# Kernel optimization log

Measured on AMD Instinct MI355X. Metric: run time of the kernel, lower is better.

## Reference

```python
import jax, jax.numpy as jnp
import numpy as np

B, T, E = 4, 2048, 512
H, D = 8, 64  # num_heads, head_dim


def setup_inputs() -> dict:
    key = jax.random.key(0)
    ks = jax.random.split(key, 9)
    s_in = 1.0 / np.sqrt(E)
    s_pr = 1.0 / np.sqrt(H * D)
    return {
        "x": jax.random.normal(ks[0], (B, T, E), dtype=jnp.float32),
        "Wq": jax.random.uniform(ks[1], (H, E, D), jnp.float32, -s_in, s_in),
        "bq": jax.random.uniform(ks[2], (H, D), jnp.float32, -s_in, s_in),
        "Wk": jax.random.uniform(ks[3], (H, E, D), jnp.float32, -s_in, s_in),
        "bk": jax.random.uniform(ks[4], (H, D), jnp.float32, -s_in, s_in),
        "Wv": jax.random.uniform(ks[5], (H, E, D), jnp.float32, -s_in, s_in),
        "bv": jax.random.uniform(ks[6], (H, D), jnp.float32, -s_in, s_in),
        "Wp": jax.random.uniform(ks[7], (H * D, E), jnp.float32, -s_pr, s_pr),
        "bp": jax.random.uniform(ks[8], (E,), jnp.float32, -s_pr, s_pr),
    }


def reference(x, Wq, bq, Wk, bk, Wv, bv, Wp, bp):
    # Per-head projections, vectorized over heads: [B,T,E] x [H,E,D] -> [B,H,T,D]
    Q = jnp.einsum('bte,hed->bhtd', x, Wq) + bq[None, :, None, :]
    K = jnp.einsum('bte,hed->bhtd', x, Wk) + bk[None, :, None, :]
    V = jnp.einsum('bte,hed->bhtd', x, Wv) + bv[None, :, None, :]
    scale = 1.0 / jnp.sqrt(jnp.float32(D))
    att = jnp.einsum('bhtd,bhsd->bhts', Q, K) * scale  # [B,H,T,T]
    causal = jnp.tril(jnp.ones((T, T), dtype=bool))
    att = jnp.where(causal[None, None], att, -jnp.inf)
    att = jax.nn.softmax(att, axis=-1)
    out = jnp.einsum('bhts,bhsd->bhtd', att, V)  # [B,H,T,D]
    # concat heads: [B,T,H*D]
    out = out.transpose(0, 2, 1, 3).reshape(B, T, H * D)
    return out @ Wp + bp
```

## Files before the change

### kernel.cpp

```cpp
#include <hip/hip_runtime.h>
#include <hip/hip_bf16.h>

typedef unsigned short u16;
typedef __bf16 bf16x8 __attribute__((ext_vector_type(8)));
typedef float f32x4 __attribute__((ext_vector_type(4)));

#define B_ 4
#define T_ 2048
#define E_ 512
#define H_ 8
#define D_ 64
#define M_ (B_*T_)
#define NQKV (3*H_*D_)

__device__ __forceinline__ u16 f2b(float f) {
  unsigned u = __float_as_uint(f);
  return (u16)((u + 0x7fffu + ((u >> 16) & 1u)) >> 16);
}

__device__ __forceinline__ void gl_lds16(const void* g, void* l) {
  __builtin_amdgcn_global_load_lds((const __attribute__((address_space(1))) void*)g,
                                   (__attribute__((address_space(3))) void*)l, 16, 0, 0);
}

__global__ void k_prep(const float* __restrict__ x, u16* __restrict__ xb,
                       const float* __restrict__ Wq, const float* __restrict__ Wk,
                       const float* __restrict__ Wv, u16* __restrict__ wt,
                       const float* __restrict__ Wp, u16* __restrict__ wpT) {
  int bid = blockIdx.x;
  if (bid < 4096) {
    int i = bid * 256 + threadIdx.x;
    float4 v = reinterpret_cast<const float4*>(x)[i];
    uint2 o;
    o.x = (unsigned)f2b(v.x) | ((unsigned)f2b(v.y) << 16);
    o.y = (unsigned)f2b(v.z) | ((unsigned)f2b(v.w) << 16);
    reinterpret_cast<uint2*>(xb)[i] = o;
  } else if (bid < 7168) {
    int i = (bid - 4096) * 256 + threadIdx.x;
    int nn = i >> 9, e = i & 511;
    int qkv = nn >> 9, hd = nn & 511;
    int h = hd >> 6, d = hd & 63;
    const float* W = (qkv == 0) ? Wq : (qkv == 1) ? Wk : Wv;
    wt[i] = f2b(W[((size_t)h * E_ + e) * D_ + d]);
  } else {
    int i = (bid - 7168) * 256 + threadIdx.x;
    int e2 = i >> 9, c = i & 511;
    wpT[i] = f2b(Wp[(size_t)c * E_ + e2]);
  }
}

__global__ __launch_bounds__(256) void k_qkv_gemm(
    const u16* __restrict__ xb, const u16* __restrict__ wt,
    const float* __restrict__ bq, const float* __restrict__ bk, const float* __restrict__ bv,
    u16* __restrict__ Q, u16* __restrict__ K, u16* __restrict__ Vt)
{
  __shared__ alignas(16) u16 As[2][128 * 64];
  __shared__ alignas(16) u16 Bs[2][128 * 64];
  const int tid = threadIdx.x;
  const int lane = tid & 63;
  const int wr = (tid >> 6) >> 1, wc = (tid >> 6) & 1;
  const int rowA = blockIdx.x * 128;
  const int rowB = blockIdx.y * 128;

#define STG(bufi, kt) { \
    _Pragma("unroll") \
    for (int it = 0; it < 4; ++it) { \
      int rr = it * 32 + (tid >> 3); int cc = (kt) * 64 + (tid & 7) * 8; \
      gl_lds16(xb + (size_t)(rowA + rr) * E_ + cc, &As[bufi][it * 2048 + tid * 8]); \
      gl_lds16(wt + (size_t)(rowB + rr) * E_ + cc, &Bs[bufi][it * 2048 + tid * 8]); \
    } }

  f32x4 acc[4][4] = {};
  STG(0, 0);
  __syncthreads();
  int cur = 0;
  for (int kt = 0; kt < 8; ++kt) {
    if (kt < 7) STG(cur ^ 1, kt + 1);
    #pragma unroll
    for (int kk = 0; kk < 2; ++kk) {
      bf16x8 a[4], b[4];
      #pragma unroll
      for (int m = 0; m < 4; ++m)
        a[m] = *(const bf16x8*)&As[cur][(wr * 64 + m * 16 + (lane & 15)) * 64 + kk * 32 + (lane >> 4) * 8];
      #pragma unroll
      for (int n = 0; n < 4; ++n)
        b[n] = *(const bf16x8*)&Bs[cur][(wc * 64 + n * 16 + (lane & 15)) * 64 + kk * 32 + (lane >> 4) * 8];
      #pragma unroll
      for (int m = 0; m < 4; ++m)
        #pragma unroll
        for (int n = 0; n < 4; ++n)
          acc[m][n] = __builtin_amdgcn_mfma_f32_16x16x32_bf16(a[m], b[n], acc[m][n], 0, 0, 0);
    }
    __syncthreads();
    cur ^= 1;
  }

  const int col0 = rowB + wc * 64;
  const int r0 = rowA + wr * 64;
  #pragma unroll
  for (int n = 0; n < 4; ++n) {
    int col = col0 + n * 16 + (lane & 15);
    int qkv = col >> 9;
    int hd = col & 511;
    int h = hd >> 6, d = hd & 63;
    const float* bias = (qkv == 0) ? bq : (qkv == 1) ? bk : bv;
    float bb = bias[hd];
    float sc = (qkv == 0) ? 0.125f : 1.0f;
    #pragma unroll
    for (int m = 0; m < 4; ++m) {
      int r = r0 + m * 16 + ((lane >> 4) << 2);
      int b = r >> 11, t = r & 2047;
      if (qkv == 2) {
        uint2 val;
        val.x = (unsigned)f2b(acc[m][n][0] + bb) | ((unsigned)f2b(acc[m][n][1] + bb) << 16);
        val.y = (unsigned)f2b(acc[m][n][2] + bb) | ((unsigned)f2b(acc[m][n][3] + bb) << 16);
        *reinterpret_cast<uint2*>(&Vt[(((size_t)(b * H_ + h) * D_ + d) * T_) + t]) = val;
      } else {
        u16* dst = (qkv == 0) ? Q : K;
        #pragma unroll
        for (int j = 0; j < 4; ++j)
          dst[(((size_t)(b * H_ + h) * T_) + t + j) * D_ + d] = f2b((acc[m][n][j] + bb) * sc);
      }
    }
  }
#undef STG
}

__global__ __launch_bounds__(256) void k_attn(
    const u16* __restrict__ Q, const u16* __restrict__ K,
    const u16* __restrict__ Vt, u16* __restrict__ O)
{
  __shared__ alignas(16) u16 Ks[2][64 * 64];
  __shared__ alignas(16) u16 Vs[2][64 * 64];
  __shared__ alignas(16) u16 Ps[4][16 * 64];
  const int tid = threadIdx.x, lane = tid & 63, w = tid >> 6;
  const int cl = lane & 15, g = lane >> 4;
  const int qp = blockIdx.x >> 5;
  const int bh = blockIdx.x & 31;
  const size_t base = (size_t)bh * T_ * D_;
  const int b = bh >> 3, h = bh & 7;

  bf16x8 vone;
  #pragma unroll
  for (int i = 0; i < 8; ++i) vone[i] = (__bf16)1.0f;

#define STGKV(bufi, kt) { \
    _Pragma("unroll") \
    for (int it = 0; it < 2; ++it) { \
      int rr = it * 32 + (tid >> 3); \
      int csw = (((tid & 7) ^ (rr & 7))) * 8; \
      gl_lds16(K  + base + (size_t)((kt) * 64 + rr) * D_ + csw, &Ks[bufi][it * 2048 + tid * 8]); \
      gl_lds16(Vt + base + (size_t)rr * T_ + (kt) * 64 + csw,   &Vs[bufi][it * 2048 + tid * 8]); \
    } }

  #pragma unroll 1
  for (int half = 0; half < 2; ++half) {
    const int qt = half ? (31 - qp) : qp;
    const int nt = qt + 1;
    const int qrow0 = qt * 64 + w * 16;

    bf16x8 aq[2];
    #pragma unroll
    for (int kk = 0; kk < 2; ++kk)
      aq[kk] = *(const bf16x8*)&Q[base + (size_t)(qrow0 + cl) * D_ + kk * 32 + g * 8];

    f32x4 acc_o[4] = {};
    f32x4 acc_l = {0.f, 0.f, 0.f, 0.f};

    STGKV(0, 0);
    __syncthreads();
    int cur = 0;
    for (int kt = 0; kt < nt; ++kt) {
      if (kt + 1 < nt) STGKV(cur ^ 1, kt + 1);
      f32x4 s[4] = {};
      #pragma unroll
      for (int kk = 0; kk < 2; ++kk) {
        bf16x8 bk_[4];
        #pragma unroll
        for (int n = 0; n < 4; ++n)
          bk_[n] = *(const bf16x8*)&Ks[cur][(n * 16 + cl) * 64 + (((kk * 4 + g) ^ (cl & 7)) << 3)];
        #pragma unroll
        for (int n = 0; n < 4; ++n)
          s[n] = __builtin_amdgcn_mfma_f32_16x16x32_bf16(aq[kk], bk_[n], s[n], 0, 0, 0);
      }
      const bool diag = (kt == qt);
      float pexp[4][4];
      #pragma unroll
      for (int n = 0; n < 4; ++n)
        #pragma unroll
        for (int j = 0; j < 4; ++j) {
          float v = s[n][j];
          if (diag) {
            int colr = n * 16 + cl;
            int rowr = w * 16 + (g << 2) + j;
            v = (colr <= rowr) ? v : -1e30f;
          }
          pexp[n][j] = __expf(v);
        }
      #pragma unroll
      for (int n = 0; n < 4; ++n)
        #pragma unroll
        for (int j = 0; j < 4; ++j) {
          int r = (g << 2) + j;
          int col = n * 16 + cl;
          Ps[w][r * 64 + (((col >> 3) ^ (r & 7)) << 3) + (col & 7)] = f2b(pexp[n][j]);
        }
      #pragma unroll
      for (int kk = 0; kk < 2; ++kk) {
        bf16x8 ap = *(const bf16x8*)&Ps[w][cl * 64 + (((kk * 4 + g) ^ (cl & 7)) << 3)];
        bf16x8 bv_[4];
        #pragma unroll
        for (int n = 0; n < 4; ++n)
          bv_[n] = *(const bf16x8*)&Vs[cur][(n * 16 + cl) * 64 + (((kk * 4 + g) ^ (cl & 7)) << 3)];
        #pragma unroll
        for (int n = 0; n < 4; ++n)
          acc_o[n] = __builtin_amdgcn_mfma_f32_16x16x32_bf16(ap, bv_[n], acc_o[n], 0, 0, 0);
        acc_l = __builtin_amdgcn_mfma_f32_16x16x32_bf16(ap, vone, acc_l, 0, 0, 0);
      }
      __syncthreads();
      cur ^= 1;
    }

    #pragma unroll
    for (int n = 0; n < 4; ++n)
      #pragma unroll
      for (int j = 0; j < 4; ++j) {
        int t = qrow0 + (g << 2) + j;
        O[((size_t)(b * T_ + t)) * E_ + h * 64 + n * 16 + cl] = f2b(acc_o[n][j] / acc_l[j]);
      }
  }
#undef STGKV
}

__global__ __launch_bounds__(256) void k_oproj(
    const u16* __restrict__ A, const u16* __restrict__ Wt,
    const float* __restrict__ bp, float* __restrict__ outp)
{
  __shared__ alignas(16) u16 As[2][128 * 64];
  __shared__ alignas(16) u16 Bs[2][128 * 64];
  const int tid = threadIdx.x;
  const int lane = tid & 63;
  const int wr = (tid >> 6) >> 1, wc = (tid >> 6) & 1;
  const int rowA = blockIdx.x * 128;
  const int rowB = blockIdx.y * 128;

#define STG(bufi, kt) { \
    _Pragma("unroll") \
    for (int it = 0; it < 4; ++it) { \
      int rr = it * 32 + (tid >> 3); int cc = (kt) * 64 + (tid & 7) * 8; \
      gl_lds16(A  + (size_t)(rowA + rr) * E_ + cc, &As[bufi][it * 2048 + tid * 8]); \
      gl_lds16(Wt + (size_t)(rowB + rr) * E_ + cc, &Bs[bufi][it * 2048 + tid * 8]); \
    } }

  f32x4 acc[4][4] = {};
  STG(0, 0);
  __syncthreads();
  int cur = 0;
  for (int kt = 0; kt < 8; ++kt) {
    if (kt < 7) STG(cur ^ 1, kt + 1);
    #pragma unroll
    for (int kk = 0; kk < 2; ++kk) {
      bf16x8 a[4], b[4];
      #pragma unroll
      for (int m = 0; m < 4; ++m)
        a[m] = *(const bf16x8*)&As[cur][(wr * 64 + m * 16 + (lane & 15)) * 64 + kk * 32 + (lane >> 4) * 8];
      #pragma unroll
      for (int n = 0; n < 4; ++n)
        b[n] = *(const bf16x8*)&Bs[cur][(wc * 64 + n * 16 + (lane & 15)) * 64 + kk * 32 + (lane >> 4) * 8];
      #pragma unroll
      for (int m = 0; m < 4; ++m)
        #pragma unroll
        for (int n = 0; n < 4; ++n)
          acc[m][n] = __builtin_amdgcn_mfma_f32_16x16x32_bf16(a[m], b[n], acc[m][n], 0, 0, 0);
    }
    __syncthreads();
    cur ^= 1;
  }

  const int col0 = rowB + wc * 64;
  const int r0 = rowA + wr * 64;
  #pragma unroll
  for (int n = 0; n < 4; ++n) {
    int col = col0 + n * 16 + (lane & 15);
    float bb = bp[col];
    #pragma unroll
    for (int m = 0; m < 4; ++m)
      #pragma unroll
      for (int j = 0; j < 4; ++j) {
        int r = r0 + m * 16 + ((lane >> 4) << 2) + j;
        outp[(size_t)r * E_ + col] = acc[m][n][j] + bb;
      }
  }
#undef STG
}

extern "C" void kernel_launch(void* const* d_in, const int* in_sizes, int n_in,
                              void* d_out, int out_size, void* d_ws, size_t ws_size,
                              hipStream_t stream) {
  (void)in_sizes; (void)n_in; (void)out_size; (void)ws_size;
  const float* x  = (const float*)d_in[0];
  const float* Wq = (const float*)d_in[1];
  const float* bq = (const float*)d_in[2];
  const float* Wk = (const float*)d_in[3];
  const float* bk = (const float*)d_in[4];
  const float* Wv = (const float*)d_in[5];
  const float* bv = (const float*)d_in[6];
  const float* Wp = (const float*)d_in[7];
  const float* bp = (const float*)d_in[8];
  float* outp = (float*)d_out;

  char* ws = (char*)d_ws;
  size_t o = 0;
  u16* xb  = (u16*)(ws + o); o += (size_t)M_ * E_ * 2;
  u16* wt  = (u16*)(ws + o); o += (size_t)NQKV * E_ * 2;
  u16* wpT = (u16*)(ws + o); o += (size_t)E_ * E_ * 2;
  u16* Qb  = (u16*)(ws + o); o += (size_t)B_ * H_ * T_ * D_ * 2;
  u16* Kb  = (u16*)(ws + o); o += (size_t)B_ * H_ * T_ * D_ * 2;
  u16* Vtb = (u16*)(ws + o); o += (size_t)B_ * H_ * T_ * D_ * 2;
  u16* Ob  = xb;

  k_prep<<<8192, 256, 0, stream>>>(x, xb, Wq, Wk, Wv, wt, Wp, wpT);
  k_qkv_gemm<<<dim3(M_ / 128, NQKV / 128), 256, 0, stream>>>(xb, wt, bq, bk, bv, Qb, Kb, Vtb);
  k_attn<<<512, 256, 0, stream>>>(Qb, Kb, Vtb, Ob);
  k_oproj<<<dim3(M_ / 128, E_ / 128), 256, 0, stream>>>(Ob, wpT, bp, outp);
}
```

Before: 165.8 us.

## Use 128-row query tiles with 8 waves and exp2 with a folded log2e scale

```diff
diff --git a/kernel.cpp b/kernel.cpp
--- a/kernel.cpp
+++ b/kernel.cpp
@@ -105,7 +105,7 @@
     int h = hd >> 6, d = hd & 63;
     const float* bias = (qkv == 0) ? bq : (qkv == 1) ? bk : bv;
     float bb = bias[hd];
-    float sc = (qkv == 0) ? 0.125f : 1.0f;
+    float sc = (qkv == 0) ? 0.18033688011111912f : 1.0f;
     #pragma unroll
     for (int m = 0; m < 4; ++m) {
       int r = r0 + m * 16 + ((lane >> 4) << 2);
@@ -126,109 +126,103 @@
 #undef STG
 }
 
-__global__ __launch_bounds__(256) void k_attn(
+__global__ __launch_bounds__(512) void k_attn(
     const u16* __restrict__ Q, const u16* __restrict__ K,
     const u16* __restrict__ Vt, u16* __restrict__ O)
 {
   __shared__ alignas(16) u16 Ks[2][64 * 64];
   __shared__ alignas(16) u16 Vs[2][64 * 64];
-  __shared__ alignas(16) u16 Ps[4][16 * 64];
+  __shared__ alignas(16) u16 Ps[8][16 * 64];
   const int tid = threadIdx.x, lane = tid & 63, w = tid >> 6;
   const int cl = lane & 15, g = lane >> 4;
-  const int qp = blockIdx.x >> 5;
-  const int bh = blockIdx.x & 31;
+  const int id = blockIdx.x;
+  const int bh = id & 31;
+  const int qh = id >> 5;
+  const int qt = (qh < 8) ? qh : (23 - qh);
   const size_t base = (size_t)bh * T_ * D_;
   const int b = bh >> 3, h = bh & 7;
+  const int nt = 2 * qt + 2;
+  const int qrow0 = qt * 128 + w * 16;
 
   bf16x8 vone;
   #pragma unroll
   for (int i = 0; i < 8; ++i) vone[i] = (__bf16)1.0f;
 
 #define STGKV(bufi, kt) { \
-    _Pragma("unroll") \
-    for (int it = 0; it < 2; ++it) { \
-      int rr = it * 32 + (tid >> 3); \
-      int csw = (((tid & 7) ^ (rr & 7))) * 8; \
-      gl_lds16(K  + base + (size_t)((kt) * 64 + rr) * D_ + csw, &Ks[bufi][it * 2048 + tid * 8]); \
-      gl_lds16(Vt + base + (size_t)rr * T_ + (kt) * 64 + csw,   &Vs[bufi][it * 2048 + tid * 8]); \
-    } }
-
-  #pragma unroll 1
-  for (int half = 0; half < 2; ++half) {
-    const int qt = half ? (31 - qp) : qp;
-    const int nt = qt + 1;
-    const int qrow0 = qt * 64 + w * 16;
-
-    bf16x8 aq[2];
-    #pragma unroll
-    for (int kk = 0; kk < 2; ++kk)
-      aq[kk] = *(const bf16x8*)&Q[base + (size_t)(qrow0 + cl) * D_ + kk * 32 + g * 8];
-
-    f32x4 acc_o[4] = {};
-    f32x4 acc_l = {0.f, 0.f, 0.f, 0.f};
-
-    STGKV(0, 0);
+    int rr = tid >> 3; \
+    int csw = ((tid & 7) ^ (rr & 7)) * 8; \
+    gl_lds16(K  + base + (size_t)((kt) * 64 + rr) * D_ + csw, &Ks[bufi][tid * 8]); \
+    gl_lds16(Vt + base + (size_t)rr * T_ + (kt) * 64 + csw,   &Vs[bufi][tid * 8]); }
+
+  bf16x8 aq[2];
+  #pragma unroll
+  for (int kk = 0; kk < 2; ++kk)
+    aq[kk] = *(const bf16x8*)&Q[base + (size_t)(qrow0 + cl) * D_ + kk * 32 + g * 8];
+
+  f32x4 acc_o[4] = {};
+  f32x4 acc_l = {0.f, 0.f, 0.f, 0.f};
+
+  STGKV(0, 0);
+  __syncthreads();
+  int cur = 0;
+  for (int kt = 0; kt < nt; ++kt) {
+    if (kt + 1 < nt) STGKV(cur ^ 1, kt + 1);
+    f32x4 s[4] = {};
+    #pragma unroll
+    for (int kk = 0; kk < 2; ++kk) {
+      bf16x8 bk_[4];
+      #pragma unroll
+      for (int n = 0; n < 4; ++n)
+        bk_[n] = *(const bf16x8*)&Ks[cur][(n * 16 + cl) * 64 + (((kk * 4 + g) ^ (cl & 7)) << 3)];
+      #pragma unroll
+      for (int n = 0; n < 4; ++n)
+        s[n] = __builtin_amdgcn_mfma_f32_16x16x32_bf16(aq[kk], bk_[n], s[n], 0, 0, 0);
+    }
+    const bool diag = (kt * 64 + 63 > qrow0);
+    float pexp[4][4];
+    #pragma unroll
+    for (int n = 0; n < 4; ++n)
+      #pragma unroll
+      for (int j = 0; j < 4; ++j) {
+        float v = s[n][j];
+        if (diag) {
+          int scol = kt * 64 + n * 16 + cl;
+          int srow = qrow0 + (g << 2) + j;
+          v = (scol <= srow) ? v : -1e30f;
+        }
+        pexp[n][j] = __builtin_amdgcn_exp2f(v);
+      }
+    #pragma unroll
+    for (int n = 0; n < 4; ++n)
+      #pragma unroll
+      for (int j = 0; j < 4; ++j) {
+        int r = (g << 2) + j;
+        int col = n * 16 + cl;
+        Ps[w][r * 64 + (((col >> 3) ^ (r & 7)) << 3) + (col & 7)] = f2b(pexp[n][j]);
+      }
+    #pragma unroll
+    for (int kk = 0; kk < 2; ++kk) {
+      bf16x8 ap = *(const bf16x8*)&Ps[w][cl * 64 + (((kk * 4 + g) ^ (cl & 7)) << 3)];
+      bf16x8 bv_[4];
+      #pragma unroll
+      for (int n = 0; n < 4; ++n)
+        bv_[n] = *(const bf16x8*)&Vs[cur][(n * 16 + cl) * 64 + (((kk * 4 + g) ^ (cl & 7)) << 3)];
+      #pragma unroll
+      for (int n = 0; n < 4; ++n)
+        acc_o[n] = __builtin_amdgcn_mfma_f32_16x16x32_bf16(ap, bv_[n], acc_o[n], 0, 0, 0);
+      acc_l = __builtin_amdgcn_mfma_f32_16x16x32_bf16(ap, vone, acc_l, 0, 0, 0);
+    }
     __syncthreads();
-    int cur = 0;
-    for (int kt = 0; kt < nt; ++kt) {
-      if (kt + 1 < nt) STGKV(cur ^ 1, kt + 1);
-      f32x4 s[4] = {};
-      #pragma unroll
-      for (int kk = 0; kk < 2; ++kk) {
-        bf16x8 bk_[4];
-        #pragma unroll
-        for (int n = 0; n < 4; ++n)
-          bk_[n] = *(const bf16x8*)&Ks[cur][(n * 16 + cl) * 64 + (((kk * 4 + g) ^ (cl & 7)) << 3)];
-        #pragma unroll
-        for (int n = 0; n < 4; ++n)
-          s[n] = __builtin_amdgcn_mfma_f32_16x16x32_bf16(aq[kk], bk_[n], s[n], 0, 0, 0);
-      }
-      const bool diag = (kt == qt);
-      float pexp[4][4];
-      #pragma unroll
-      for (int n = 0; n < 4; ++n)
-        #pragma unroll
-        for (int j = 0; j < 4; ++j) {
-          float v = s[n][j];
-          if (diag) {
-            int colr = n * 16 + cl;
-            int rowr = w * 16 + (g << 2) + j;
-            v = (colr <= rowr) ? v : -1e30f;
-          }
-          pexp[n][j] = __expf(v);
-        }
-      #pragma unroll
-      for (int n = 0; n < 4; ++n)
-        #pragma unroll
-        for (int j = 0; j < 4; ++j) {
-          int r = (g << 2) + j;
-          int col = n * 16 + cl;
-          Ps[w][r * 64 + (((col >> 3) ^ (r & 7)) << 3) + (col & 7)] = f2b(pexp[n][j]);
-        }
-      #pragma unroll
-      for (int kk = 0; kk < 2; ++kk) {
-        bf16x8 ap = *(const bf16x8*)&Ps[w][cl * 64 + (((kk * 4 + g) ^ (cl & 7)) << 3)];
-        bf16x8 bv_[4];
-        #pragma unroll
-        for (int n = 0; n < 4; ++n)
-          bv_[n] = *(const bf16x8*)&Vs[cur][(n * 16 + cl) * 64 + (((kk * 4 + g) ^ (cl & 7)) << 3)];
-        #pragma unroll
-        for (int n = 0; n < 4; ++n)
-          acc_o[n] = __builtin_amdgcn_mfma_f32_16x16x32_bf16(ap, bv_[n], acc_o[n], 0, 0, 0);
-        acc_l = __builtin_amdgcn_mfma_f32_16x16x32_bf16(ap, vone, acc_l, 0, 0, 0);
-      }
-      __syncthreads();
-      cur ^= 1;
-    }
-
-    #pragma unroll
-    for (int n = 0; n < 4; ++n)
-      #pragma unroll
-      for (int j = 0; j < 4; ++j) {
-        int t = qrow0 + (g << 2) + j;
-        O[((size_t)(b * T_ + t)) * E_ + h * 64 + n * 16 + cl] = f2b(acc_o[n][j] / acc_l[j]);
-      }
-  }
+    cur ^= 1;
+  }
+
+  #pragma unroll
+  for (int n = 0; n < 4; ++n)
+    #pragma unroll
+    for (int j = 0; j < 4; ++j) {
+      int t = qrow0 + (g << 2) + j;
+      O[((size_t)(b * T_ + t)) * E_ + h * 64 + n * 16 + cl] = f2b(acc_o[n][j] / acc_l[j]);
+    }
 #undef STGKV
 }
 
@@ -321,6 +315,6 @@
 
   k_prep<<<8192, 256, 0, stream>>>(x, xb, Wq, Wk, Wv, wt, Wp, wpT);
   k_qkv_gemm<<<dim3(M_ / 128, NQKV / 128), 256, 0, stream>>>(xb, wt, bq, bk, bv, Qb, Kb, Vtb);
-  k_attn<<<512, 256, 0, stream>>>(Qb, Kb, Vtb, Ob);
+  k_attn<<<512, 512, 0, stream>>>(Qb, Kb, Vtb, Ob);
   k_oproj<<<dim3(M_ / 128, E_ / 128), 256, 0, stream>>>(Ob, wpT, bp, outp);
 }
```

Result: no change. 168.4 us (+1.5%).

## Stage 128-key K/V tiles per barrier and fold log2e into Q scale for exp2

Applied to the files above, without the earlier changes.

```diff
diff --git a/kernel.cpp b/kernel.cpp
--- a/kernel.cpp
+++ b/kernel.cpp
@@ -105,7 +105,7 @@
     int h = hd >> 6, d = hd & 63;
     const float* bias = (qkv == 0) ? bq : (qkv == 1) ? bk : bv;
     float bb = bias[hd];
-    float sc = (qkv == 0) ? 0.125f : 1.0f;
+    float sc = (qkv == 0) ? 0.18033688011111912f : 1.0f;
     #pragma unroll
     for (int m = 0; m < 4; ++m) {
       int r = r0 + m * 16 + ((lane >> 4) << 2);
@@ -130,8 +130,8 @@
     const u16* __restrict__ Q, const u16* __restrict__ K,
     const u16* __restrict__ Vt, u16* __restrict__ O)
 {
-  __shared__ alignas(16) u16 Ks[2][64 * 64];
-  __shared__ alignas(16) u16 Vs[2][64 * 64];
+  __shared__ alignas(16) u16 Ks[2][128 * 64];
+  __shared__ alignas(16) u16 Vs[2][64 * 128];
   __shared__ alignas(16) u16 Ps[4][16 * 64];
   const int tid = threadIdx.x, lane = tid & 63, w = tid >> 6;
   const int cl = lane & 15, g = lane >> 4;
@@ -146,17 +146,19 @@
 
 #define STGKV(bufi, kt) { \
     _Pragma("unroll") \
-    for (int it = 0; it < 2; ++it) { \
-      int rr = it * 32 + (tid >> 3); \
-      int csw = (((tid & 7) ^ (rr & 7))) * 8; \
-      gl_lds16(K  + base + (size_t)((kt) * 64 + rr) * D_ + csw, &Ks[bufi][it * 2048 + tid * 8]); \
-      gl_lds16(Vt + base + (size_t)rr * T_ + (kt) * 64 + csw,   &Vs[bufi][it * 2048 + tid * 8]); \
+    for (int it = 0; it < 4; ++it) { \
+      int rk = it * 32 + (tid >> 3); \
+      int ck = ((tid & 7) ^ (rk & 7)) * 8; \
+      gl_lds16(K + base + (size_t)((kt) * 128 + rk) * D_ + ck, &Ks[bufi][it * 2048 + tid * 8]); \
+      int rv = it * 16 + (tid >> 4); \
+      int cv = ((tid & 15) ^ (rv & 7)) * 8; \
+      gl_lds16(Vt + base + (size_t)rv * T_ + (kt) * 128 + cv, &Vs[bufi][it * 2048 + tid * 8]); \
     } }
 
   #pragma unroll 1
   for (int half = 0; half < 2; ++half) {
     const int qt = half ? (31 - qp) : qp;
-    const int nt = qt + 1;
+    const int nt = qt / 2 + 1;
     const int qrow0 = qt * 64 + w * 16;
 
     bf16x8 aq[2];
@@ -172,50 +174,55 @@
     int cur = 0;
     for (int kt = 0; kt < nt; ++kt) {
       if (kt + 1 < nt) STGKV(cur ^ 1, kt + 1);
-      f32x4 s[4] = {};
-      #pragma unroll
-      for (int kk = 0; kk < 2; ++kk) {
-        bf16x8 bk_[4];
+      #pragma unroll
+      for (int sub = 0; sub < 2; ++sub) {
+        const int colbase = kt * 128 + sub * 64;
+        if (colbase > qrow0 + 15) break;
+        f32x4 s[4] = {};
+        #pragma unroll
+        for (int kk = 0; kk < 2; ++kk) {
+          bf16x8 bk_[4];
+          #pragma unroll
+          for (int n = 0; n < 4; ++n)
+            bk_[n] = *(const bf16x8*)&Ks[cur][(sub * 64 + n * 16 + cl) * 64 + (((kk * 4 + g) ^ (cl & 7)) << 3)];
+          #pragma unroll
+          for (int n = 0; n < 4; ++n)
+            s[n] = __builtin_amdgcn_mfma_f32_16x16x32_bf16(aq[kk], bk_[n], s[n], 0, 0, 0);
+        }
+        const bool diag = (colbase + 63 > qrow0);
+        float pexp[4][4];
         #pragma unroll
         for (int n = 0; n < 4; ++n)
-          bk_[n] = *(const bf16x8*)&Ks[cur][(n * 16 + cl) * 64 + (((kk * 4 + g) ^ (cl & 7)) << 3)];
+          #pragma unroll
+          for (int j = 0; j < 4; ++j) {
+            float v = s[n][j];
+            if (diag) {
+              int scol = colbase + n * 16 + cl;
+              int srow = qrow0 + (g << 2) + j;
+              v = (scol <= srow) ? v : -1e30f;
+            }
+            pexp[n][j] = __builtin_amdgcn_exp2f(v);
+          }
         #pragma unroll
         for (int n = 0; n < 4; ++n)
-          s[n] = __builtin_amdgcn_mfma_f32_16x16x32_bf16(aq[kk], bk_[n], s[n], 0, 0, 0);
-      }
-      const bool diag = (kt == qt);
-      float pexp[4][4];
-      #pragma unroll
-      for (int n = 0; n < 4; ++n)
-        #pragma unroll
-        for (int j = 0; j < 4; ++j) {
-          float v = s[n][j];
-          if (diag) {
-            int colr = n * 16 + cl;
-            int rowr = w * 16 + (g << 2) + j;
-            v = (colr <= rowr) ? v : -1e30f;
+          #pragma unroll
+          for (int j = 0; j < 4; ++j) {
+            int r = (g << 2) + j;
+            int col = n * 16 + cl;
+            Ps[w][r * 64 + (((col >> 3) ^ (r & 7)) << 3) + (col & 7)] = f2b(pexp[n][j]);
           }
-          pexp[n][j] = __expf(v);
+        #pragma unroll
+        for (int kk = 0; kk < 2; ++kk) {
+          bf16x8 ap = *(const bf16x8*)&Ps[w][cl * 64 + (((kk * 4 + g) ^ (cl & 7)) << 3)];
+          bf16x8 bv_[4];
+          #pragma unroll
+          for (int n = 0; n < 4; ++n)
+            bv_[n] = *(const bf16x8*)&Vs[cur][(n * 16 + cl) * 128 + ((sub * 8 + ((kk * 4 + g) ^ (cl & 7))) << 3)];
+          #pragma unroll
+          for (int n = 0; n < 4; ++n)
+            acc_o[n] = __builtin_amdgcn_mfma_f32_16x16x32_bf16(ap, bv_[n], acc_o[n], 0, 0, 0);
+          acc_l = __builtin_amdgcn_mfma_f32_16x16x32_bf16(ap, vone, acc_l, 0, 0, 0);
         }
-      #pragma unroll
-      for (int n = 0; n < 4; ++n)
-        #pragma unroll
-        for (int j = 0; j < 4; ++j) {
-          int r = (g << 2) + j;
-          int col = n * 16 + cl;
-          Ps[w][r * 64 + (((col >> 3) ^ (r & 7)) << 3) + (col & 7)] = f2b(pexp[n][j]);
-        }
-      #pragma unroll
-      for (int kk = 0; kk < 2; ++kk) {
-        bf16x8 ap = *(const bf16x8*)&Ps[w][cl * 64 + (((kk * 4 + g) ^ (cl & 7)) << 3)];
-        bf16x8 bv_[4];
-        #pragma unroll
-        for (int n = 0; n < 4; ++n)
-          bv_[n] = *(const bf16x8*)&Vs[cur][(n * 16 + cl) * 64 + (((kk * 4 + g) ^ (cl & 7)) << 3)];
-        #pragma unroll
-        for (int n = 0; n < 4; ++n)
-          acc_o[n] = __builtin_amdgcn_mfma_f32_16x16x32_bf16(ap, bv_[n], acc_o[n], 0, 0, 0);
-        acc_l = __builtin_amdgcn_mfma_f32_16x16x32_bf16(ap, vone, acc_l, 0, 0, 0);
       }
       __syncthreads();
       cur ^= 1;
```

Result: slower. 169.2 us (+2.0%).
